# Performance work log

Measured on AMD Instinct MI355X. Metric: run time of the kernel, lower is better.

Reference implementation:

```python
import jax, jax.numpy as jnp
import numpy as np

B, N, D, T = 32, 512, 128, 8
NEG_SLOPE = 0.2
MASK_VAL = -1e10


def _xavier(key, shape, gain=1.0):
    fan_in, fan_out = shape[0], int(np.prod(shape[1:]))
    limit = gain * np.sqrt(6.0 / (fan_in + fan_out))
    return jax.random.uniform(key, shape, jnp.float32, -limit, limit)


def setup_inputs() -> dict:
    key = jax.random.key(0)
    ks = jax.random.split(key, 8)
    atom_embeddings = jax.random.normal(ks[0], (B, N, D), dtype=jnp.float32)
    # bond types in [-1, T-1]; -1 = no bond (masked)
    edges = jax.random.randint(ks[1], (B, N, N), 0, T + 1, dtype=jnp.int64) - 1
    Qw = _xavier(ks[2], (D, D))
    Kw = _xavier(ks[3], (D, D))
    Vw = _xavier(ks[4], (D, D))
    Pw = _xavier(ks[5], (D, D))
    Qb = jnp.zeros((D,), jnp.float32)
    Kb = jnp.zeros((D,), jnp.float32)
    Vb = jnp.zeros((D,), jnp.float32)
    Pb = jnp.zeros((D,), jnp.float32)
    a = _xavier(ks[6], (D, D, T), gain=1.414)
    return {"atom_embeddings": atom_embeddings, "edges": edges,
            "Qw": Qw, "Qb": Qb, "Kw": Kw, "Kb": Kb, "Vw": Vw, "Vb": Vb,
            "a": a, "Pw": Pw, "Pb": Pb}


def reference(atom_embeddings, edges, Qw, Qb, Kw, Kb, Vw, Vb, a, Pw, Pb):
    # torch Linear: x @ W.T + b
    src = atom_embeddings @ Qw.T + Qb            # (B,N,D)
    dst = atom_embeddings @ Kw.T + Kb            # (B,N,D)
    val = atom_embeddings @ Vw.T + Vb            # (B,N,D)

    # bilinear edge-type scores: s[b,n,m,t] = src[b,n,:] @ a[:,:,t] @ dst[b,m,:]
    ts = jnp.einsum('bnd,det->bnet', src, a)     # (B,N,D,T)
    scores = jnp.einsum('bnet,bme->bnmt', ts, dst)  # (B,N,N,T)

    # gather the slice for each edge's bond type (clamp -1 -> 0 like torch)
    idx = jnp.clip(edges, 0, None)[..., None]    # (B,N,N,1)
    att = jnp.take_along_axis(scores, idx, axis=-1)[..., 0]  # (B,N,N)
    att = jnp.where(edges == -1, MASK_VAL, att)
    att = jnp.where(att >= 0, att, NEG_SLOPE * att)  # leaky_relu
    att = jax.nn.softmax(att, axis=-1)           # (B,N,N)

    out = att @ val                              # (B,N,D)
    return out @ Pw.T + Pb
```

## Files before the change

kernel.cpp:

```cpp
#include <hip/hip_runtime.h>
#include <stdint.h>


typedef short bf16x8 __attribute__((ext_vector_type(8)));
typedef float f32x4 __attribute__((ext_vector_type(4)));
typedef unsigned short u16;
typedef unsigned int u32;

__device__ __forceinline__ u16 f2bf(float x) {
    union { float f; u32 u; } v; v.f = x;
    u32 r = v.u + 0x7FFFu + ((v.u >> 16) & 1u);
    return (u16)(r >> 16);
}
__device__ __forceinline__ float bf2f(u16 h) {
    union { u32 u; float f; } v; v.u = ((u32)h) << 16; return v.f;
}
__device__ __forceinline__ void split_hl(float x, u16& h, u16& l) {
    h = f2bf(x);
    l = f2bf(x - bf2f(h));
}
__device__ __forceinline__ f32x4 mfma16(bf16x8 a, bf16x8 b, f32x4 c) {
    return __builtin_amdgcn_mfma_f32_16x16x32_bf16(a, b, c, 0, 0, 0);
}

__global__ void prep_kernel(const float* __restrict__ Qw, const float* __restrict__ Qb,
                            const float* __restrict__ Kw, const float* __restrict__ Kb,
                            const float* __restrict__ Vw, const float* __restrict__ Vb,
                            const float* __restrict__ Aa, const float* __restrict__ Pw,
                            u16* __restrict__ WH, u16* __restrict__ WL,
                            float* __restrict__ bcat) {
    int gid = blockIdx.x * 256 + threadIdx.x;
    if (gid >= 1280 * 128) return;
    int j = gid >> 7, d = gid & 127;
    float v, bias = 0.f;
    if (j < 128) { v = Kw[j * 128 + d]; bias = Kb[j]; }
    else if (j < 256) {
        int jj = j - 128;
        float s = 0.f, bs = 0.f;
        for (int k = 0; k < 128; k++) {
            float p = Pw[jj * 128 + k];
            s += p * Vw[k * 128 + d];
            bs += p * Vb[k];
        }
        v = s; bias = bs;
    } else {
        int r = j - 256, t = r >> 7, jj = r & 127;
        float s = 0.f, bs = 0.f;
        for (int e = 0; e < 128; e++) {
            float av = Aa[(e * 128 + jj) * 8 + t];
            s += Qw[e * 128 + d] * av;
            bs += Qb[e] * av;
        }
        v = s; bias = bs;
    }
    u16 h, l; split_hl(v, h, l);
    WH[gid] = h; WL[gid] = l;
    if (d == 0) bcat[j] = bias;
}

__global__ void detect_kernel(const int* __restrict__ E, int* __restrict__ flag) {
    __shared__ int bad;
    if (threadIdx.x == 0) bad = 0;
    __syncthreads();
    int w0 = E[2 * threadIdx.x + 1];
    int w1 = E[2 * (threadIdx.x + 256) + 1];
    if (!(w0 == 0 || w0 == -1) || !(w1 == 0 || w1 == -1)) atomicOr(&bad, 1);
    __syncthreads();
    if (threadIdx.x == 0) *flag = (bad ? 0 : 1);
}

__global__ void econv_kernel(const void* __restrict__ E, const int* __restrict__ flag,
                             signed char* __restrict__ E8) {
    int i = (blockIdx.x * 256 + threadIdx.x) * 4;
    char4 o;
    if (*flag) {
        const long long* p = (const long long*)E;
        o.x = (signed char)p[i]; o.y = (signed char)p[i + 1];
        o.z = (signed char)p[i + 2]; o.w = (signed char)p[i + 3];
    } else {
        const int* p = (const int*)E;
        o.x = (signed char)p[i]; o.y = (signed char)p[i + 1];
        o.z = (signed char)p[i + 2]; o.w = (signed char)p[i + 3];
    }
    *(char4*)(E8 + i) = o;
}

__launch_bounds__(256, 2)
__global__ void gemm1_kernel(const float* __restrict__ X,
                             const u16* __restrict__ WH, const u16* __restrict__ WL,
                             const float* __restrict__ bcat,
                             u16* __restrict__ CH, u16* __restrict__ CL,
                             u16* __restrict__ VTH, u16* __restrict__ VTL) {
    const int id = blockIdx.x;
    const int xcd = id & 7, q5 = id >> 3;
    const int g0 = (xcd * 32 + (q5 >> 1)) * 64;
    const int jbase = (q5 & 1) * 10;
    __shared__ u16 WB[2][2][64 * 128];
    const int tid = threadIdx.x;
    const int wid = tid >> 6, lane = tid & 63;
    const int wr = (wid >> 1) * 32, wc = (wid & 1) * 32;
    const int lr = lane & 15, lg = lane >> 4;

    {
        const float4* Xv = (const float4*)(X + (size_t)g0 * 128);
        #pragma unroll
        for (int i = 0; i < 8; i++) {
            int idx = tid + i * 256;
            float4 x = Xv[idx];
            int row = idx >> 5, c4 = idx & 31;
            int boff = (row * 256 + c4 * 8) ^ ((row & 7) << 4);
            u16* ph = (u16*)((char*)WB[1][0] + boff);
            u16* pl = (u16*)((char*)WB[1][1] + boff);
            const float* xf = (const float*)&x;
            #pragma unroll
            for (int qq = 0; qq < 4; qq++) { u16 h, l; split_hl(xf[qq], h, l); ph[qq] = h; pl[qq] = l; }
        }
    }
    uint4 nh[4], nl[4];
    {
        const uint4* bh = (const uint4*)(WH + (size_t)(jbase + 0) * 64 * 128);
        const uint4* bl = (const uint4*)(WL + (size_t)(jbase + 0) * 64 * 128);
        #pragma unroll
        for (int i = 0; i < 4; i++) { nh[i] = bh[tid + i * 256]; nl[i] = bl[tid + i * 256]; }
    }
    __syncthreads();
    bf16x8 afh[4][2], afl[4][2];
    #pragma unroll
    for (int ks = 0; ks < 4; ks++) {
        const int kb2 = (ks * 32 + lg * 8) * 2;
        #pragma unroll
        for (int r = 0; r < 2; r++) {
            int row = wr + r * 16 + lr;
            int boff = (row * 256 + kb2) ^ ((row & 7) << 4);
            afh[ks][r] = *(const bf16x8*)((const char*)WB[1][0] + boff);
            afl[ks][r] = *(const bf16x8*)((const char*)WB[1][1] + boff);
        }
    }
    #pragma unroll
    for (int i = 0; i < 4; i++) {
        int idx = tid + i * 256;
        int row = idx >> 4, ch = idx & 15;
        int boff = (row * 256 + ch * 16) ^ ((row & 7) << 4);
        *(uint4*)((char*)WB[0][0] + boff) = nh[i];
        *(uint4*)((char*)WB[0][1] + boff) = nl[i];
    }

    for (int jt = 0; jt < 10; jt++) {
        __syncthreads();
        if (jt < 9) {
            const uint4* bh = (const uint4*)(WH + (size_t)(jbase + jt + 1) * 64 * 128);
            const uint4* bl = (const uint4*)(WL + (size_t)(jbase + jt + 1) * 64 * 128);
            #pragma unroll
            for (int i = 0; i < 4; i++) { nh[i] = bh[tid + i * 256]; nl[i] = bl[tid + i * 256]; }
        }
        const int cur = jt & 1;
        f32x4 acc[2][2] = {};
        #pragma unroll
        for (int ks = 0; ks < 4; ks++) {
            const int kb2 = (ks * 32 + lg * 8) * 2;
            bf16x8 bfh[2], bfl[2];
            #pragma unroll
            for (int c = 0; c < 2; c++) {
                int row = wc + c * 16 + lr;
                int boff = (row * 256 + kb2) ^ ((row & 7) << 4);
                bfh[c] = *(const bf16x8*)((const char*)WB[cur][0] + boff);
                bfl[c] = *(const bf16x8*)((const char*)WB[cur][1] + boff);
            }
            #pragma unroll
            for (int r = 0; r < 2; r++)
            #pragma unroll
            for (int c = 0; c < 2; c++) {
                acc[r][c] = mfma16(afh[ks][r], bfh[c], acc[r][c]);
                acc[r][c] = mfma16(afh[ks][r], bfl[c], acc[r][c]);
                acc[r][c] = mfma16(afl[ks][r], bfh[c], acc[r][c]);
            }
        }
        const int j0 = (jbase + jt) * 64;
        const bool valTile = (j0 >= 128 && j0 < 256);
        #pragma unroll
        for (int r = 0; r < 2; r++)
        #pragma unroll
        for (int c = 0; c < 2; c++) {
            int j = j0 + wc + c * 16 + lr;
            float bias = bcat[j];
            #pragma unroll
            for (int qq = 0; qq < 4; qq++) {
                int g1 = g0 + wr + r * 16 + 4 * lg + qq;
                float v = acc[r][c][qq] + bias;
                u16 h, l; split_hl(v, h, l);
                if (valTile) {
                    int bb = g1 >> 9, n = g1 & 511;
                    size_t off = ((size_t)(bb * 128 + (j - 128))) * 512 + n;
                    VTH[off] = h; VTL[off] = l;
                } else {
                    size_t off = (size_t)g1 * 1280 + j;
                    CH[off] = h; CL[off] = l;
                }
            }
        }
        if (jt < 9) {
            #pragma unroll
            for (int i = 0; i < 4; i++) {
                int idx = tid + i * 256;
                int row = idx >> 4, ch = idx & 15;
                int boff = (row * 256 + ch * 16) ^ ((row & 7) << 4);
                *(uint4*)((char*)WB[cur ^ 1][0] + boff) = nh[i];
                *(uint4*)((char*)WB[cur ^ 1][1] + boff) = nl[i];
            }
        }
    }
}

__launch_bounds__(512, 2)
__global__ void scores_kernel(const u16* __restrict__ CH, const u16* __restrict__ CL,
                              const signed char* __restrict__ E8,
                              float* __restrict__ att) {
    const int id = blockIdx.x;
    const int xcd = id & 7, j = id >> 3;
    const int m0 = (j & 3) * 128;
    const int pair = xcd * 32 + (j >> 2);
    const int n0 = (pair & 7) * 64, b = pair >> 3;
    __shared__ u16 BH[128 * 128], BL[128 * 128];
    __shared__ u16 AH[2][64 * 128], AL[2][64 * 128];
    const int tid = threadIdx.x;
    const int wid = tid >> 6, lane = tid & 63;
    const int wr = (wid >> 2) * 32, wc = (wid & 3) * 32;
    const int lr = lane & 15, lg = lane >> 4;

    #pragma unroll
    for (int i = 0; i < 4; i++) {
        int idx = tid + i * 512;
        int row = idx >> 4, ch = idx & 15;
        size_t src = (size_t)(b * 512 + m0 + row) * 1280;
        int boff = (row * 256 + ch * 16) ^ ((row & 7) << 4);
        *(uint4*)((char*)BH + boff) = ((const uint4*)(CH + src))[ch];
        *(uint4*)((char*)BL + boff) = ((const uint4*)(CL + src))[ch];
    }
    int ed[2][2][4];
    #pragma unroll
    for (int r = 0; r < 2; r++)
    #pragma unroll
    for (int c = 0; c < 2; c++)
    #pragma unroll
    for (int q = 0; q < 4; q++) {
        int n = n0 + wr + r * 16 + 4 * lg + q;
        int m = m0 + wc + c * 16 + lr;
        ed[r][c][q] = E8[((size_t)b * 512 + n) * 512 + m];
    }
    uint4 rh[2], rl[2];
    {
        #pragma unroll
        for (int i = 0; i < 2; i++) {
            int idx = tid + i * 512;
            int row = idx >> 4, ch = idx & 15;
            size_t src = (size_t)(b * 512 + n0 + row) * 1280 + 256;
            rh[i] = ((const uint4*)(CH + src))[ch];
            rl[i] = ((const uint4*)(CL + src))[ch];
        }
        #pragma unroll
        for (int i = 0; i < 2; i++) {
            int idx = tid + i * 512;
            int row = idx >> 4, ch = idx & 15;
            int boff = (row * 256 + ch * 16) ^ ((row & 7) << 4);
            *(uint4*)((char*)AH[0] + boff) = rh[i];
            *(uint4*)((char*)AL[0] + boff) = rl[i];
        }
    }
    __syncthreads();
    bf16x8 bfh[4][2], bfl[4][2];
    #pragma unroll
    for (int ks = 0; ks < 4; ks++) {
        const int kb2 = (ks * 32 + lg * 8) * 2;
        #pragma unroll
        for (int c = 0; c < 2; c++) {
            int row = wc + c * 16 + lr;
            int boff = (row * 256 + kb2) ^ ((row & 7) << 4);
            bfh[ks][c] = *(const bf16x8*)((const char*)BH + boff);
            bfl[ks][c] = *(const bf16x8*)((const char*)BL + boff);
        }
    }
    float sel[2][2][4];
    #pragma unroll
    for (int r = 0; r < 2; r++)
    #pragma unroll
    for (int c = 0; c < 2; c++)
    #pragma unroll
    for (int q = 0; q < 4; q++) sel[r][c][q] = 0.f;

    for (int t = 0; t < 8; t++) {
        const int cur = t & 1;
        uint4 nh[2], nl[2];
        if (t < 7) {
            #pragma unroll
            for (int i = 0; i < 2; i++) {
                int idx = tid + i * 512;
                int row = idx >> 4, ch = idx & 15;
                size_t src = (size_t)(b * 512 + n0 + row) * 1280 + 256 + (t + 1) * 128;
                nh[i] = ((const uint4*)(CH + src))[ch];
                nl[i] = ((const uint4*)(CL + src))[ch];
            }
        }
        f32x4 acc[2][2] = {};
        #pragma unroll
        for (int ks = 0; ks < 4; ks++) {
            const int kb2 = (ks * 32 + lg * 8) * 2;
            bf16x8 afh[2], afl[2];
            #pragma unroll
            for (int r = 0; r < 2; r++) {
                int row = wr + r * 16 + lr;
                int boff = (row * 256 + kb2) ^ ((row & 7) << 4);
                afh[r] = *(const bf16x8*)((const char*)AH[cur] + boff);
                afl[r] = *(const bf16x8*)((const char*)AL[cur] + boff);
            }
            #pragma unroll
            for (int r = 0; r < 2; r++)
            #pragma unroll
            for (int c = 0; c < 2; c++) {
                acc[r][c] = mfma16(afh[r], bfh[ks][c], acc[r][c]);
                acc[r][c] = mfma16(afh[r], bfl[ks][c], acc[r][c]);
                acc[r][c] = mfma16(afl[r], bfh[ks][c], acc[r][c]);
            }
        }
        #pragma unroll
        for (int r = 0; r < 2; r++)
        #pragma unroll
        for (int c = 0; c < 2; c++)
        #pragma unroll
        for (int q = 0; q < 4; q++) {
            int ec = ed[r][c][q] < 0 ? 0 : ed[r][c][q];
            sel[r][c][q] = (ec == t) ? acc[r][c][q] : sel[r][c][q];
        }
        if (t < 7) {
            #pragma unroll
            for (int i = 0; i < 2; i++) {
                int idx = tid + i * 512;
                int row = idx >> 4, ch = idx & 15;
                int boff = (row * 256 + ch * 16) ^ ((row & 7) << 4);
                *(uint4*)((char*)AH[cur ^ 1] + boff) = nh[i];
                *(uint4*)((char*)AL[cur ^ 1] + boff) = nl[i];
            }
        }
        __syncthreads();
    }
    #pragma unroll
    for (int r = 0; r < 2; r++)
    #pragma unroll
    for (int c = 0; c < 2; c++)
    #pragma unroll
    for (int q = 0; q < 4; q++) {
        float v = (ed[r][c][q] == -1) ? -1e10f : sel[r][c][q];
        v = (v >= 0.f) ? v : 0.2f * v;
        size_t n = n0 + wr + r * 16 + 4 * lg + q;
        size_t m = m0 + wc + c * 16 + lr;
        att[((size_t)b * 512 + n) * 512 + m] = v;
    }
}

__launch_bounds__(256, 2)
__global__ void out_kernel(const float* __restrict__ att,
                           const u16* __restrict__ VTH, const u16* __restrict__ VTL,
                           const float* __restrict__ Pb, float* __restrict__ out) {
    const int id = blockIdx.x;
    const int xcd = id & 7, j = id >> 3;
    const int b = xcd * 4 + (j >> 4);
    const int n0 = (j & 15) * 32;
    __shared__ u16 PH[32 * 64], PL[32 * 64];
    __shared__ u16 VH[128 * 64], VL[128 * 64];
    const int tid = threadIdx.x;
    const int row = tid >> 3, c8 = tid & 7;
    float4 av0[8], av1[8];
    const float4* rp = (const float4*)(att + ((size_t)b * 512 + n0 + row) * 512);
    #pragma unroll
    for (int mc = 0; mc < 8; mc++) {
        av0[mc] = rp[mc * 16 + c8 * 2];
        av1[mc] = rp[mc * 16 + c8 * 2 + 1];
    }
    float mx = -1e30f;
    #pragma unroll
    for (int mc = 0; mc < 8; mc++) {
        mx = fmaxf(mx, fmaxf(fmaxf(fmaxf(av0[mc].x, av0[mc].y), fmaxf(av0[mc].z, av0[mc].w)),
                             fmaxf(fmaxf(av1[mc].x, av1[mc].y), fmaxf(av1[mc].z, av1[mc].w))));
    }
    #pragma unroll
    for (int o = 1; o < 8; o <<= 1) mx = fmaxf(mx, __shfl_xor(mx, o, 64));
    float s = 0.f;
    #pragma unroll
    for (int mc = 0; mc < 8; mc++) {
        av0[mc].x = expf(av0[mc].x - mx); av0[mc].y = expf(av0[mc].y - mx);
        av0[mc].z = expf(av0[mc].z - mx); av0[mc].w = expf(av0[mc].w - mx);
        av1[mc].x = expf(av1[mc].x - mx); av1[mc].y = expf(av1[mc].y - mx);
        av1[mc].z = expf(av1[mc].z - mx); av1[mc].w = expf(av1[mc].w - mx);
        s += av0[mc].x + av0[mc].y + av0[mc].z + av0[mc].w
           + av1[mc].x + av1[mc].y + av1[mc].z + av1[mc].w;
    }
    #pragma unroll
    for (int o = 1; o < 8; o <<= 1) s += __shfl_xor(s, o, 64);
    const float inv = 1.0f / s;
    const int wid = tid >> 6, lane = tid & 63;
    const int lr = lane & 15, lg = lane >> 4;
    const int wc = wid * 32;
    f32x4 acc[2][2] = {};
    for (int mc = 0; mc < 8; mc++) {
        {
            union { u16 us[8]; uint4 v; } uh, ul;
            float xs0 = av0[mc].x * inv, xs1 = av0[mc].y * inv;
            float xs2 = av0[mc].z * inv, xs3 = av0[mc].w * inv;
            float xs4 = av1[mc].x * inv, xs5 = av1[mc].y * inv;
            float xs6 = av1[mc].z * inv, xs7 = av1[mc].w * inv;
            split_hl(xs0, uh.us[0], ul.us[0]); split_hl(xs1, uh.us[1], ul.us[1]);
            split_hl(xs2, uh.us[2], ul.us[2]); split_hl(xs3, uh.us[3], ul.us[3]);
            split_hl(xs4, uh.us[4], ul.us[4]); split_hl(xs5, uh.us[5], ul.us[5]);
            split_hl(xs6, uh.us[6], ul.us[6]); split_hl(xs7, uh.us[7], ul.us[7]);
            int boff = (row * 128 + c8 * 16) ^ ((row & 7) << 4);
            *(uint4*)((char*)PH + boff) = uh.v;
            *(uint4*)((char*)PL + boff) = ul.v;
        }
        #pragma unroll
        for (int i = 0; i < 4; i++) {
            int idx = tid + i * 256;
            int vrow = idx >> 3, ch = idx & 7;
            size_t src = ((size_t)(b * 128 + vrow)) * 512 + mc * 64;
            int boff = (vrow * 128 + ch * 16) ^ ((vrow & 7) << 4);
            *(uint4*)((char*)VH + boff) = ((const uint4*)(VTH + src))[ch];
            *(uint4*)((char*)VL + boff) = ((const uint4*)(VTL + src))[ch];
        }
        __syncthreads();
        #pragma unroll
        for (int ks = 0; ks < 2; ks++) {
            const int kb2 = (ks * 32 + lg * 8) * 2;
            bf16x8 ah[2], al[2];
            #pragma unroll
            for (int r = 0; r < 2; r++) {
                int prow = r * 16 + lr;
                int boff = (prow * 128 + kb2) ^ ((prow & 7) << 4);
                ah[r] = *(const bf16x8*)((const char*)PH + boff);
                al[r] = *(const bf16x8*)((const char*)PL + boff);
            }
            #pragma unroll
            for (int c = 0; c < 2; c++) {
                int vrow = wc + c * 16 + lr;
                int boff = (vrow * 128 + kb2) ^ ((vrow & 7) << 4);
                bf16x8 bh = *(const bf16x8*)((const char*)VH + boff);
                bf16x8 bl = *(const bf16x8*)((const char*)VL + boff);
                #pragma unroll
                for (int r = 0; r < 2; r++) {
                    acc[r][c] = mfma16(ah[r], bh, acc[r][c]);
                    acc[r][c] = mfma16(ah[r], bl, acc[r][c]);
                    acc[r][c] = mfma16(al[r], bh, acc[r][c]);
                }
            }
        }
        __syncthreads();
    }
    #pragma unroll
    for (int r = 0; r < 2; r++)
    #pragma unroll
    for (int c = 0; c < 2; c++)
    #pragma unroll
    for (int q = 0; q < 4; q++) {
        int n = n0 + r * 16 + 4 * lg + q;
        int d = wc + c * 16 + lr;
        out[((size_t)b * 512 + n) * 128 + d] = acc[r][c][q] + Pb[d];
    }
}

extern "C" void kernel_launch(void* const* d_in, const int* in_sizes, int n_in,
                              void* d_out, int out_size, void* d_ws, size_t ws_size,
                              hipStream_t stream) {
    (void)in_sizes; (void)n_in; (void)out_size; (void)ws_size;
    const float* X  = (const float*)d_in[0];
    const void*  E  = d_in[1];
    const float* Qw = (const float*)d_in[2];
    const float* Qb = (const float*)d_in[3];
    const float* Kw = (const float*)d_in[4];
    const float* Kb = (const float*)d_in[5];
    const float* Vw = (const float*)d_in[6];
    const float* Vb = (const float*)d_in[7];
    const float* Aa = (const float*)d_in[8];
    const float* Pw = (const float*)d_in[9];
    const float* Pb = (const float*)d_in[10];
    float* out = (float*)d_out;

    char* ws = (char*)d_ws;
    size_t cur = 0;
    auto alloc = [&](size_t bytes) -> char* {
        char* p = ws + cur;
        cur += (bytes + 255) & ~(size_t)255;
        return p;
    };
    int*   flag = (int*)  alloc(4);
    u16*   WH   = (u16*)  alloc((size_t)1280 * 128 * 2);
    u16*   WL   = (u16*)  alloc((size_t)1280 * 128 * 2);
    float* bcat = (float*)alloc(1280 * 4);
    u16*   CH   = (u16*)  alloc((size_t)16384 * 1280 * 2);
    u16*   CL   = (u16*)  alloc((size_t)16384 * 1280 * 2);
    u16*   VTH  = (u16*)  alloc((size_t)32 * 128 * 512 * 2);
    u16*   VTL  = (u16*)  alloc((size_t)32 * 128 * 512 * 2);
    float* att  = (float*)alloc((size_t)32 * 512 * 512 * 4);
    signed char* E8 = (signed char*)alloc((size_t)32 * 512 * 512);

    prep_kernel<<<640, 256, 0, stream>>>(Qw, Qb, Kw, Kb, Vw, Vb, Aa, Pw, WH, WL, bcat);
    detect_kernel<<<1, 256, 0, stream>>>((const int*)E, flag);
    econv_kernel<<<8192, 256, 0, stream>>>(E, flag, E8);
    gemm1_kernel<<<512, 256, 0, stream>>>(X, WH, WL, bcat, CH, CL, VTH, VTL);
    scores_kernel<<<1024, 512, 0, stream>>>(CH, CL, E8, att);
    out_kernel<<<512, 256, 0, stream>>>(att, VTH, VTL, Pb, out);
}
```

Measured before the change: 250.2 us.

## Store projection output as fp32 and split hi/lo in scores kernel

```diff
diff --git a/kernel.cpp b/kernel.cpp
--- a/kernel.cpp
+++ b/kernel.cpp
@@ -6,6 +6,7 @@
 typedef float f32x4 __attribute__((ext_vector_type(4)));
 typedef unsigned short u16;
 typedef unsigned int u32;
+typedef unsigned long long u64;
 
 __device__ __forceinline__ u16 f2bf(float x) {
     union { float f; u32 u; } v; v.f = x;
@@ -18,6 +19,13 @@
 __device__ __forceinline__ void split_hl(float x, u16& h, u16& l) {
     h = f2bf(x);
     l = f2bf(x - bf2f(h));
+}
+__device__ __forceinline__ void split4(float4 x, u64& hq, u64& lq) {
+    u16 h0, l0, h1, l1, h2, l2, h3, l3;
+    split_hl(x.x, h0, l0); split_hl(x.y, h1, l1);
+    split_hl(x.z, h2, l2); split_hl(x.w, h3, l3);
+    hq = (u64)h0 | ((u64)h1 << 16) | ((u64)h2 << 32) | ((u64)h3 << 48);
+    lq = (u64)l0 | ((u64)l1 << 16) | ((u64)l2 << 32) | ((u64)l3 << 48);
 }
 __device__ __forceinline__ f32x4 mfma16(bf16x8 a, bf16x8 b, f32x4 c) {
     return __builtin_amdgcn_mfma_f32_16x16x32_bf16(a, b, c, 0, 0, 0);
@@ -89,7 +97,7 @@
 __global__ void gemm1_kernel(const float* __restrict__ X,
                              const u16* __restrict__ WH, const u16* __restrict__ WL,
                              const float* __restrict__ bcat,
-                             u16* __restrict__ CH, u16* __restrict__ CL,
+                             float* __restrict__ C,
                              u16* __restrict__ VTH, u16* __restrict__ VTL) {
     const int id = blockIdx.x;
     const int xcd = id & 7, q5 = id >> 3;
@@ -98,7 +106,7 @@
     __shared__ u16 WB[2][2][64 * 128];
     const int tid = threadIdx.x;
     const int wid = tid >> 6, lane = tid & 63;
-    const int wr = (wid >> 1) * 32, wc = (wid & 1) * 32;
+    const int gblk = (wid >> 1) * 32, jblk = (wid & 1) * 32;
     const int lr = lane & 15, lg = lane >> 4;
 
     {
@@ -109,11 +117,9 @@
             float4 x = Xv[idx];
             int row = idx >> 5, c4 = idx & 31;
             int boff = (row * 256 + c4 * 8) ^ ((row & 7) << 4);
-            u16* ph = (u16*)((char*)WB[1][0] + boff);
-            u16* pl = (u16*)((char*)WB[1][1] + boff);
-            const float* xf = (const float*)&x;
-            #pragma unroll
-            for (int qq = 0; qq < 4; qq++) { u16 h, l; split_hl(xf[qq], h, l); ph[qq] = h; pl[qq] = l; }
+            u64 hq, lq; split4(x, hq, lq);
+            *(u64*)((char*)WB[1][0] + boff) = hq;
+            *(u64*)((char*)WB[1][1] + boff) = lq;
         }
     }
     uint4 nh[4], nl[4];
@@ -130,7 +136,7 @@
         const int kb2 = (ks * 32 + lg * 8) * 2;
         #pragma unroll
         for (int r = 0; r < 2; r++) {
-            int row = wr + r * 16 + lr;
+            int row = gblk + r * 16 + lr;
             int boff = (row * 256 + kb2) ^ ((row & 7) << 4);
             afh[ks][r] = *(const bf16x8*)((const char*)WB[1][0] + boff);
             afl[ks][r] = *(const bf16x8*)((const char*)WB[1][1] + boff);
@@ -154,48 +160,78 @@
             for (int i = 0; i < 4; i++) { nh[i] = bh[tid + i * 256]; nl[i] = bl[tid + i * 256]; }
         }
         const int cur = jt & 1;
-        f32x4 acc[2][2] = {};
-        #pragma unroll
-        for (int ks = 0; ks < 4; ks++) {
-            const int kb2 = (ks * 32 + lg * 8) * 2;
-            bf16x8 bfh[2], bfl[2];
-            #pragma unroll
-            for (int c = 0; c < 2; c++) {
-                int row = wc + c * 16 + lr;
-                int boff = (row * 256 + kb2) ^ ((row & 7) << 4);
-                bfh[c] = *(const bf16x8*)((const char*)WB[cur][0] + boff);
-                bfl[c] = *(const bf16x8*)((const char*)WB[cur][1] + boff);
-            }
-            #pragma unroll
-            for (int r = 0; r < 2; r++)
-            #pragma unroll
-            for (int c = 0; c < 2; c++) {
-                acc[r][c] = mfma16(afh[ks][r], bfh[c], acc[r][c]);
-                acc[r][c] = mfma16(afh[ks][r], bfl[c], acc[r][c]);
-                acc[r][c] = mfma16(afl[ks][r], bfh[c], acc[r][c]);
-            }
-        }
         const int j0 = (jbase + jt) * 64;
         const bool valTile = (j0 >= 128 && j0 < 256);
-        #pragma unroll
-        for (int r = 0; r < 2; r++)
-        #pragma unroll
-        for (int c = 0; c < 2; c++) {
-            int j = j0 + wc + c * 16 + lr;
-            float bias = bcat[j];
-            #pragma unroll
-            for (int qq = 0; qq < 4; qq++) {
-                int g1 = g0 + wr + r * 16 + 4 * lg + qq;
-                float v = acc[r][c][qq] + bias;
-                u16 h, l; split_hl(v, h, l);
-                if (valTile) {
-                    int bb = g1 >> 9, n = g1 & 511;
-                    size_t off = ((size_t)(bb * 128 + (j - 128))) * 512 + n;
-                    VTH[off] = h; VTL[off] = l;
-                } else {
-                    size_t off = (size_t)g1 * 1280 + j;
-                    CH[off] = h; CL[off] = l;
+        f32x4 acc[2][2] = {};
+        if (valTile) {
+            #pragma unroll
+            for (int ks = 0; ks < 4; ks++) {
+                const int kb2 = (ks * 32 + lg * 8) * 2;
+                bf16x8 bfh[2], bfl[2];
+                #pragma unroll
+                for (int c = 0; c < 2; c++) {
+                    int row = jblk + c * 16 + lr;
+                    int boff = (row * 256 + kb2) ^ ((row & 7) << 4);
+                    bfh[c] = *(const bf16x8*)((const char*)WB[cur][0] + boff);
+                    bfl[c] = *(const bf16x8*)((const char*)WB[cur][1] + boff);
                 }
+                #pragma unroll
+                for (int r = 0; r < 2; r++)
+                #pragma unroll
+                for (int c = 0; c < 2; c++) {
+                    acc[r][c] = mfma16(afh[ks][r], bfh[c], acc[r][c]);
+                    acc[r][c] = mfma16(afh[ks][r], bfl[c], acc[r][c]);
+                    acc[r][c] = mfma16(afl[ks][r], bfh[c], acc[r][c]);
+                }
+            }
+            const int b = g0 >> 9;
+            #pragma unroll
+            for (int r = 0; r < 2; r++)
+            #pragma unroll
+            for (int c = 0; c < 2; c++) {
+                int j = j0 + jblk + c * 16 + lr;
+                float bias = bcat[j];
+                int d = j - 128;
+                int n = (g0 & 511) + gblk + r * 16 + 4 * lg;
+                u64 hq, lq;
+                float4 v = {acc[r][c][0] + bias, acc[r][c][1] + bias,
+                            acc[r][c][2] + bias, acc[r][c][3] + bias};
+                split4(v, hq, lq);
+                size_t off = ((size_t)(b * 128 + d)) * 512 + n;
+                *(u64*)(VTH + off) = hq;
+                *(u64*)(VTL + off) = lq;
+            }
+        } else {
+            #pragma unroll
+            for (int ks = 0; ks < 4; ks++) {
+                const int kb2 = (ks * 32 + lg * 8) * 2;
+                bf16x8 bfh[2], bfl[2];
+                #pragma unroll
+                for (int c = 0; c < 2; c++) {
+                    int row = jblk + c * 16 + lr;
+                    int boff = (row * 256 + kb2) ^ ((row & 7) << 4);
+                    bfh[c] = *(const bf16x8*)((const char*)WB[cur][0] + boff);
+                    bfl[c] = *(const bf16x8*)((const char*)WB[cur][1] + boff);
+                }
+                #pragma unroll
+                for (int c = 0; c < 2; c++)
+                #pragma unroll
+                for (int r = 0; r < 2; r++) {
+                    acc[c][r] = mfma16(bfh[c], afh[ks][r], acc[c][r]);
+                    acc[c][r] = mfma16(bfh[c], afl[ks][r], acc[c][r]);
+                    acc[c][r] = mfma16(bfl[c], afh[ks][r], acc[c][r]);
+                }
+            }
+            #pragma unroll
+            for (int c = 0; c < 2; c++)
+            #pragma unroll
+            for (int r = 0; r < 2; r++) {
+                int j = j0 + jblk + c * 16 + 4 * lg;
+                int g = g0 + gblk + r * 16 + lr;
+                float4 bias4 = *(const float4*)(bcat + j);
+                float4 v = {acc[c][r][0] + bias4.x, acc[c][r][1] + bias4.y,
+                            acc[c][r][2] + bias4.z, acc[c][r][3] + bias4.w};
+                *(float4*)(C + (size_t)g * 1280 + j) = v;
             }
         }
         if (jt < 9) {
@@ -212,7 +248,7 @@
 }
 
 __launch_bounds__(512, 2)
-__global__ void scores_kernel(const u16* __restrict__ CH, const u16* __restrict__ CL,
+__global__ void scores_kernel(const float* __restrict__ C,
                               const signed char* __restrict__ E8,
                               float* __restrict__ att) {
     const int id = blockIdx.x;
@@ -228,13 +264,14 @@
     const int lr = lane & 15, lg = lane >> 4;
 
     #pragma unroll
-    for (int i = 0; i < 4; i++) {
+    for (int i = 0; i < 8; i++) {
         int idx = tid + i * 512;
-        int row = idx >> 4, ch = idx & 15;
-        size_t src = (size_t)(b * 512 + m0 + row) * 1280;
-        int boff = (row * 256 + ch * 16) ^ ((row & 7) << 4);
-        *(uint4*)((char*)BH + boff) = ((const uint4*)(CH + src))[ch];
-        *(uint4*)((char*)BL + boff) = ((const uint4*)(CL + src))[ch];
+        int row = idx >> 5, c4 = idx & 31;
+        float4 x = *(const float4*)(C + (size_t)(b * 512 + m0 + row) * 1280 + c4 * 4);
+        u64 hq, lq; split4(x, hq, lq);
+        int boff = (row * 256 + c4 * 8) ^ ((row & 7) << 4);
+        *(u64*)((char*)BH + boff) = hq;
+        *(u64*)((char*)BL + boff) = lq;
     }
     int ed[2][2][4];
     #pragma unroll
@@ -247,23 +284,16 @@
         int m = m0 + wc + c * 16 + lr;
         ed[r][c][q] = E8[((size_t)b * 512 + n) * 512 + m];
     }
-    uint4 rh[2], rl[2];
     {
         #pragma unroll
-        for (int i = 0; i < 2; i++) {
+        for (int i = 0; i < 4; i++) {
             int idx = tid + i * 512;
-            int row = idx >> 4, ch = idx & 15;
-            size_t src = (size_t)(b * 512 + n0 + row) * 1280 + 256;
-            rh[i] = ((const uint4*)(CH + src))[ch];
-            rl[i] = ((const uint4*)(CL + src))[ch];
-        }
-        #pragma unroll
-        for (int i = 0; i < 2; i++) {
-            int idx = tid + i * 512;
-            int row = idx >> 4, ch = idx & 15;
-            int boff = (row * 256 + ch * 16) ^ ((row & 7) << 4);
-            *(uint4*)((char*)AH[0] + boff) = rh[i];
-            *(uint4*)((char*)AL[0] + boff) = rl[i];
+            int row = idx >> 5, c4 = idx & 31;
+            float4 x = *(const float4*)(C + (size_t)(b * 512 + n0 + row) * 1280 + 256 + c4 * 4);
+            u64 hq, lq; split4(x, hq, lq);
+            int boff = (row * 256 + c4 * 8) ^ ((row & 7) << 4);
+            *(u64*)((char*)AH[0] + boff) = hq;
+            *(u64*)((char*)AL[0] + boff) = lq;
         }
     }
     __syncthreads();
@@ -289,18 +319,18 @@
 
     for (int t = 0; t < 8; t++) {
         const int cur = t & 1;
-        uint4 nh[2], nl[2];
+        float4 nx[4];
         if (t < 7) {
             #pragma unroll
-            for (int i = 0; i < 2; i++) {
+            for (int i = 0; i < 4; i++) {
                 int idx = tid + i * 512;
-                int row = idx >> 4, ch = idx & 15;
-                size_t src = (size_t)(b * 512 + n0 + row) * 1280 + 256 + (t + 1) * 128;
-                nh[i] = ((const uint4*)(CH + src))[ch];
-                nl[i] = ((const uint4*)(CL + src))[ch];
+                int row = idx >> 5, c4 = idx & 31;
+                nx[i] = *(const float4*)(C + (size_t)(b * 512 + n0 + row) * 1280
+                                           + 256 + (t + 1) * 128 + c4 * 4);
             }
         }
         f32x4 acc[2][2] = {};
+        __builtin_amdgcn_s_setprio(1);
         #pragma unroll
         for (int ks = 0; ks < 4; ks++) {
             const int kb2 = (ks * 32 + lg * 8) * 2;
@@ -321,6 +351,7 @@
                 acc[r][c] = mfma16(afl[r], bfh[ks][c], acc[r][c]);
             }
         }
+        __builtin_amdgcn_s_setprio(0);
         #pragma unroll
         for (int r = 0; r < 2; r++)
         #pragma unroll
@@ -332,12 +363,13 @@
         }
         if (t < 7) {
             #pragma unroll
-            for (int i = 0; i < 2; i++) {
+            for (int i = 0; i < 4; i++) {
                 int idx = tid + i * 512;
-                int row = idx >> 4, ch = idx & 15;
-                int boff = (row * 256 + ch * 16) ^ ((row & 7) << 4);
-                *(uint4*)((char*)AH[cur ^ 1] + boff) = nh[i];
-                *(uint4*)((char*)AL[cur ^ 1] + boff) = nl[i];
+                int row = idx >> 5, c4 = idx & 31;
+                u64 hq, lq; split4(nx[i], hq, lq);
+                int boff = (row * 256 + c4 * 8) ^ ((row & 7) << 4);
+                *(u64*)((char*)AH[cur ^ 1] + boff) = hq;
+                *(u64*)((char*)AL[cur ^ 1] + boff) = lq;
             }
         }
         __syncthreads();
@@ -402,18 +434,15 @@
     f32x4 acc[2][2] = {};
     for (int mc = 0; mc < 8; mc++) {
         {
-            union { u16 us[8]; uint4 v; } uh, ul;
-            float xs0 = av0[mc].x * inv, xs1 = av0[mc].y * inv;
-            float xs2 = av0[mc].z * inv, xs3 = av0[mc].w * inv;
-            float xs4 = av1[mc].x * inv, xs5 = av1[mc].y * inv;
-            float xs6 = av1[mc].z * inv, xs7 = av1[mc].w * inv;
-            split_hl(xs0, uh.us[0], ul.us[0]); split_hl(xs1, uh.us[1], ul.us[1]);
-            split_hl(xs2, uh.us[2], ul.us[2]); split_hl(xs3, uh.us[3], ul.us[3]);
-            split_hl(xs4, uh.us[4], ul.us[4]); split_hl(xs5, uh.us[5], ul.us[5]);
-            split_hl(xs6, uh.us[6], ul.us[6]); split_hl(xs7, uh.us[7], ul.us[7]);
+            float4 p0 = {av0[mc].x * inv, av0[mc].y * inv, av0[mc].z * inv, av0[mc].w * inv};
+            float4 p1 = {av1[mc].x * inv, av1[mc].y * inv, av1[mc].z * inv, av1[mc].w * inv};
+            u64 h0, l0, h1, l1;
+            split4(p0, h0, l0); split4(p1, h1, l1);
             int boff = (row * 128 + c8 * 16) ^ ((row & 7) << 4);
-            *(uint4*)((char*)PH + boff) = uh.v;
-            *(uint4*)((char*)PL + boff) = ul.v;
+            *(u64*)((char*)PH + boff) = h0;
+            *(u64*)((char*)PH + boff + 8) = h1;
+            *(u64*)((char*)PL + boff) = l0;
+            *(u64*)((char*)PL + boff + 8) = l1;
         }
         #pragma unroll
         for (int i = 0; i < 4; i++) {
@@ -492,8 +521,7 @@
     u16*   WH   = (u16*)  alloc((size_t)1280 * 128 * 2);
     u16*   WL   = (u16*)  alloc((size_t)1280 * 128 * 2);
     float* bcat = (float*)alloc(1280 * 4);
-    u16*   CH   = (u16*)  alloc((size_t)16384 * 1280 * 2);
-    u16*   CL   = (u16*)  alloc((size_t)16384 * 1280 * 2);
+    float* C    = (float*)alloc((size_t)16384 * 1280 * 4);
     u16*   VTH  = (u16*)  alloc((size_t)32 * 128 * 512 * 2);
     u16*   VTL  = (u16*)  alloc((size_t)32 * 128 * 512 * 2);
     float* att  = (float*)alloc((size_t)32 * 512 * 512 * 4);
@@ -502,7 +530,7 @@
     prep_kernel<<<640, 256, 0, stream>>>(Qw, Qb, Kw, Kb, Vw, Vb, Aa, Pw, WH, WL, bcat);
     detect_kernel<<<1, 256, 0, stream>>>((const int*)E, flag);
     econv_kernel<<<8192, 256, 0, stream>>>(E, flag, E8);
-    gemm1_kernel<<<512, 256, 0, stream>>>(X, WH, WL, bcat, CH, CL, VTH, VTL);
-    scores_kernel<<<1024, 512, 0, stream>>>(CH, CL, E8, att);
+    gemm1_kernel<<<512, 256, 0, stream>>>(X, WH, WL, bcat, C, VTH, VTL);
+    scores_kernel<<<1024, 512, 0, stream>>>(C, E8, att);
     out_kernel<<<512, 256, 0, stream>>>(att, VTH, VTL, Pb, out);
 }
```

After: 264.3 us. 1.06x slower.
